# Performance work log

Measured on AMD Instinct MI355X. Metric: run time of the kernel, lower is better.

The kernel has to match this reference:

```python
import jax, jax.numpy as jnp
import numpy as np


def _dequantize_int4(qweight, scales, qzeros, blocksize):
    """Unpack int4 weights (two nibbles per byte along N) and dequantize.

    qweight: [K, N/2] int (byte values 0..255); low nibble = even col, high nibble = odd col
    scales:  [groups, N] float32, groups = K // blocksize
    qzeros:  [groups, N/2] int (packed like qweight)
    returns: [K, N] float32 dequantized weight, w = (q - z) * s per group along K
    """
    K, Nh = qweight.shape
    N = Nh * 2
    groups = scales.shape[0]
    low = (qweight & 0xF).astype(jnp.float32)
    high = ((qweight >> 4) & 0xF).astype(jnp.float32)
    wq = jnp.stack([low, high], axis=-1).reshape(K, N)  # [K, N]
    zl = (qzeros & 0xF).astype(jnp.float32)
    zh = ((qzeros >> 4) & 0xF).astype(jnp.float32)
    zq = jnp.stack([zl, zh], axis=-1).reshape(groups, N)  # [groups, N]
    # group-wise dequant along K without materializing repeated scale/zero tables
    w = (wq.reshape(groups, blocksize, N) - zq[:, None, :]) * scales[:, None, :]
    return w.reshape(K, N)


def setup_inputs() -> dict:
    key = jax.random.key(0)
    k1, k2, k3, k4, k5 = jax.random.split(key, 5)
    B, S, K = 32, 64, 4096
    N_PAD = 32064
    BLOCKSIZE = 128
    GROUPS = K // BLOCKSIZE
    x = jax.random.normal(k1, (B, S, K), dtype=jnp.float32)
    qweight = jax.random.randint(k2, (K, N_PAD // 2), 0, 256, dtype=jnp.int32)
    scales = jax.random.uniform(k3, (GROUPS, N_PAD), dtype=jnp.float32) * 0.02 + 1e-3
    qzeros = jax.random.randint(k4, (GROUPS, N_PAD // 2), 0, 256, dtype=jnp.int32)
    bias = jax.random.normal(k5, (N_PAD,), dtype=jnp.float32) * 0.01
    return {"x": x, "qweight": qweight, "scales": scales, "qzeros": qzeros,
            "bias": bias, "blocksize": BLOCKSIZE, "n_dim": 32000}


def reference(x, qweight, scales, qzeros, bias, blocksize, n_dim):
    # mimic module.forward with acc_test=False: keep only the last token
    if x.ndim > 3:
        x = x.reshape(-1, x.shape[-2], x.shape[-1])
    x_last = x[:, -1:, :]  # [B, 1, K]
    w = _dequantize_int4(qweight, scales, qzeros, blocksize)  # [K, N_pad]
    out = jnp.einsum('bsk,kn->bsn', x_last, w) + bias  # mm_bias_int4
    return out[:, :, :n_dim]  # strip vocab padding
```

## Files before the change

kernel.cpp:

```cpp
#include <hip/hip_runtime.h>
#include <hip/hip_bf16.h>


typedef _Float16 f16x8 __attribute__((ext_vector_type(8)));
typedef _Float16 f16x2 __attribute__((ext_vector_type(2)));
typedef float f32x4 __attribute__((ext_vector_type(4)));

#define K_DIM 4096
#define NP 16032
#define NSC 32064
#define NOUT 32000
#define S_LEN 64
#define QROWB ((size_t)NP * 4)
#define QSTEP (32u * (uint32_t)NP * 4u)

__global__ void prep_a_kernel(const float* __restrict__ x,
                              _Float16* __restrict__ aws) {
    int tid = blockIdx.x * 256 + threadIdx.x;
    int l = tid & 63;
    int mblk = (tid >> 6) & 1;
    int ks = tid >> 7;
    int m = mblk * 16 + (l & 15);
    int kbase = ks * 32 + 8 * (l >> 4);
    const float* xp = x + (size_t)m * S_LEN * K_DIM + (size_t)(S_LEN - 1) * K_DIM + kbase;
    _Float16* op = aws + (size_t)tid * 8;
#pragma unroll
    for (int j = 0; j < 8; ++j) op[j] = (_Float16)xp[j];
}

__device__ __forceinline__ int f16pk(int w0, int w1, int sh2) {
    int e0 = (w0 >> sh2) & 15;
    int e1 = (w1 >> sh2) & 15;
    return e0 | (e1 << 16) | 0x64006400;
}

__global__ __launch_bounds__(512, 4)
void q4gemm_kernel(const int* __restrict__ qw,
                   const float* __restrict__ scales,
                   const int* __restrict__ qzeros,
                   const float* __restrict__ bias,
                   const _Float16* __restrict__ aws,
                   float* __restrict__ out) {
    __shared__ float red[8 * 2048];

    const int tid = threadIdx.x;
    const int w = tid >> 6;
    const int l = tid & 63;
    const int h = l >> 4;
    const int c = l & 15;
    const int n0 = blockIdx.x * 64;
    const int np0 = n0 >> 1;

    const char* qwb = (const char*)qw;
    uint32_t qoff = (uint32_t)((w * 512 + 8 * h) * (size_t)NP + np0 + 2 * c) * 4u;

    f32x4 acc0[4] = {};
    f32x4 acc1[4] = {};
    f16x2 vz[4], vs[4];

    int2 qa[8], qb[8];

#define QLD(buf)                                                              \
    do {                                                                      \
        _Pragma("unroll") for (int j = 0; j < 8; ++j)                         \
            buf[j] = *(const int2*)(qwb + qoff + (size_t)j * QROWB);          \
        qoff += QSTEP;                                                        \
    } while (0)

#define GRPUPD(g)                                                             \
    do {                                                                      \
        f32x4 sc4 = *(const f32x4*)(scales + (size_t)(g) * NSC + n0 + 4 * c); \
        int2 zw = *(const int2*)(qzeros + (size_t)(g) * NP + np0 + 2 * c);    \
        _Pragma("unroll") for (int s = 0; s < 4; ++s) {                       \
            int zword = (s < 2) ? zw.x : zw.y;                                \
            int z = (zword >> ((s & 1) * 4)) & 15;                            \
            int zp = z | (z << 16) | 0x64006400;                              \
            vz[s] = __builtin_bit_cast(f16x2, zp);                            \
            _Float16 sh_ = (_Float16)sc4[s];                                  \
            f16x2 sp = {sh_, sh_};                                            \
            vs[s] = sp;                                                       \
        }                                                                     \
    } while (0)

#define COMPUTE(buf, ksg)                                                     \
    do {                                                                      \
        f16x8 a0 = *(const f16x8*)(aws + ((size_t)((ksg) * 2 + 0) * 64 + l) * 8); \
        f16x8 a1 = *(const f16x8*)(aws + ((size_t)((ksg) * 2 + 1) * 64 + l) * 8); \
        _Pragma("unroll") for (int s = 0; s < 4; ++s) {                       \
            const int sh2 = (s & 1) * 4;                                      \
            int4 bi;                                                          \
            _Pragma("unroll") for (int p = 0; p < 4; ++p) {                   \
                int w0 = (s < 2) ? buf[2 * p].x : buf[2 * p].y;               \
                int w1 = (s < 2) ? buf[2 * p + 1].x : buf[2 * p + 1].y;       \
                f16x2 vq = __builtin_bit_cast(f16x2, f16pk(w0, w1, sh2));     \
                f16x2 r = (vq - vz[s]) * vs[s];                               \
                bi[p] = __builtin_bit_cast(int, r);                           \
            }                                                                 \
            f16x8 b = __builtin_bit_cast(f16x8, bi);                          \
            acc0[s] = __builtin_amdgcn_mfma_f32_16x16x32_f16(a0, b, acc0[s], 0, 0, 0); \
            acc1[s] = __builtin_amdgcn_mfma_f32_16x16x32_f16(a1, b, acc1[s], 0, 0, 0); \
        }                                                                     \
    } while (0)

    QLD(qa);
#pragma unroll
    for (int tt = 0; tt < 8; ++tt) {
        const int t0 = 2 * tt;
        QLD(qb);
        if ((tt & 1) == 0) GRPUPD(w * 4 + tt / 2);
        COMPUTE(qa, w * 16 + t0);
        if (tt < 7) QLD(qa);
        COMPUTE(qb, w * 16 + t0 + 1);
    }

#pragma unroll
    for (int s = 0; s < 4; ++s)
#pragma unroll
        for (int r = 0; r < 4; ++r) {
            red[w * 2048 + (h * 4 + r) * 64 + 4 * c + s] = acc0[s][r];
            red[w * 2048 + (16 + h * 4 + r) * 64 + 4 * c + s] = acc1[s][r];
        }

    __syncthreads();

#pragma unroll
    for (int i = 0; i < 4; ++i) {
        int e = i * 512 + tid;
        float sum = 0.f;
#pragma unroll
        for (int ww = 0; ww < 8; ++ww) sum += red[ww * 2048 + e];
        int m = e >> 6;
        int n = n0 + (e & 63);
        out[(size_t)m * NOUT + n] = sum + bias[n];
    }
}

extern "C" void kernel_launch(void* const* d_in, const int* in_sizes, int n_in,
                              void* d_out, int out_size, void* d_ws, size_t ws_size,
                              hipStream_t stream) {
    const float* x       = (const float*)d_in[0];
    const int*   qweight = (const int*)d_in[1];
    const float* scales  = (const float*)d_in[2];
    const int*   qzeros  = (const int*)d_in[3];
    const float* bias    = (const float*)d_in[4];

    _Float16* aws = (_Float16*)d_ws;
    float* out = (float*)d_out;

    prep_a_kernel<<<64, 256, 0, stream>>>(x, aws);
    q4gemm_kernel<<<500, 512, 0, stream>>>(qweight, scales, qzeros, bias, aws, out);
}
```

Before: 50.16 us.

## Fuse activation fp16 conversion into GEMM kernel and use nontemporal weight loads

Drops the separate prep kernel that converted the last-token activations to fp16 in a workspace. Each GEMM wave now loads the fp32 activations directly and converts them in registers, saving one kernel launch and a workspace round trip. Weight, scale and zero loads are switched to nontemporal loads so the streamed weights do not pollute the cache. The cost is that all 500 blocks re-read and re-convert the fp32 activations, which doubles activation bytes per load and adds conversion instructions.

```diff
diff --git a/kernel.cpp b/kernel.cpp
--- a/kernel.cpp
+++ b/kernel.cpp
@@ -5,6 +5,7 @@
 typedef _Float16 f16x8 __attribute__((ext_vector_type(8)));
 typedef _Float16 f16x2 __attribute__((ext_vector_type(2)));
 typedef float f32x4 __attribute__((ext_vector_type(4)));
+typedef int i32x2 __attribute__((ext_vector_type(2)));
 
 #define K_DIM 4096
 #define NP 16032
@@ -14,32 +15,12 @@
 #define QROWB ((size_t)NP * 4)
 #define QSTEP (32u * (uint32_t)NP * 4u)
 
-__global__ void prep_a_kernel(const float* __restrict__ x,
-                              _Float16* __restrict__ aws) {
-    int tid = blockIdx.x * 256 + threadIdx.x;
-    int l = tid & 63;
-    int mblk = (tid >> 6) & 1;
-    int ks = tid >> 7;
-    int m = mblk * 16 + (l & 15);
-    int kbase = ks * 32 + 8 * (l >> 4);
-    const float* xp = x + (size_t)m * S_LEN * K_DIM + (size_t)(S_LEN - 1) * K_DIM + kbase;
-    _Float16* op = aws + (size_t)tid * 8;
-#pragma unroll
-    for (int j = 0; j < 8; ++j) op[j] = (_Float16)xp[j];
-}
-
-__device__ __forceinline__ int f16pk(int w0, int w1, int sh2) {
-    int e0 = (w0 >> sh2) & 15;
-    int e1 = (w1 >> sh2) & 15;
-    return e0 | (e1 << 16) | 0x64006400;
-}
-
 __global__ __launch_bounds__(512, 4)
-void q4gemm_kernel(const int* __restrict__ qw,
+void q4gemm_kernel(const float* __restrict__ x,
+                   const int* __restrict__ qw,
                    const float* __restrict__ scales,
                    const int* __restrict__ qzeros,
                    const float* __restrict__ bias,
-                   const _Float16* __restrict__ aws,
                    float* __restrict__ out) {
     __shared__ float red[8 * 2048];
 
@@ -54,25 +35,31 @@
     const char* qwb = (const char*)qw;
     uint32_t qoff = (uint32_t)((w * 512 + 8 * h) * (size_t)NP + np0 + 2 * c) * 4u;
 
+    const float* xr0 = x + ((size_t)c * S_LEN + (S_LEN - 1)) * K_DIM;
+    const float* xr1 = x + ((size_t)(16 + c) * S_LEN + (S_LEN - 1)) * K_DIM;
+
     f32x4 acc0[4] = {};
     f32x4 acc1[4] = {};
     f16x2 vz[4], vs[4];
 
-    int2 qa[8], qb[8];
+    i32x2 qa[8], qb[8];
 
 #define QLD(buf)                                                              \
     do {                                                                      \
         _Pragma("unroll") for (int j = 0; j < 8; ++j)                         \
-            buf[j] = *(const int2*)(qwb + qoff + (size_t)j * QROWB);          \
+            buf[j] = __builtin_nontemporal_load(                              \
+                (const i32x2*)(qwb + qoff + (size_t)j * QROWB));              \
         qoff += QSTEP;                                                        \
     } while (0)
 
 #define GRPUPD(g)                                                             \
     do {                                                                      \
-        f32x4 sc4 = *(const f32x4*)(scales + (size_t)(g) * NSC + n0 + 4 * c); \
-        int2 zw = *(const int2*)(qzeros + (size_t)(g) * NP + np0 + 2 * c);    \
+        f32x4 sc4 = __builtin_nontemporal_load(                               \
+            (const f32x4*)(scales + (size_t)(g) * NSC + n0 + 4 * c));         \
+        i32x2 zw = __builtin_nontemporal_load(                                \
+            (const i32x2*)(qzeros + (size_t)(g) * NP + np0 + 2 * c));         \
         _Pragma("unroll") for (int s = 0; s < 4; ++s) {                       \
-            int zword = (s < 2) ? zw.x : zw.y;                                \
+            int zword = (s < 2) ? zw[0] : zw[1];                              \
             int z = (zword >> ((s & 1) * 4)) & 15;                            \
             int zp = z | (z << 16) | 0x64006400;                              \
             vz[s] = __builtin_bit_cast(f16x2, zp);                            \
@@ -82,17 +69,32 @@
         }                                                                     \
     } while (0)
 
+#define AFRAG(dst, xr, koff)                                                  \
+    do {                                                                      \
+        f32x4 u0 = *(const f32x4*)((xr) + (koff));                            \
+        f32x4 u1 = *(const f32x4*)((xr) + (koff) + 4);                        \
+        _Pragma("unroll") for (int j = 0; j < 4; ++j) {                       \
+            dst[j] = (_Float16)u0[j];                                         \
+            dst[4 + j] = (_Float16)u1[j];                                     \
+        }                                                                     \
+    } while (0)
+
 #define COMPUTE(buf, ksg)                                                     \
     do {                                                                      \
-        f16x8 a0 = *(const f16x8*)(aws + ((size_t)((ksg) * 2 + 0) * 64 + l) * 8); \
-        f16x8 a1 = *(const f16x8*)(aws + ((size_t)((ksg) * 2 + 1) * 64 + l) * 8); \
+        const int koff = (ksg) * 32 + 8 * h;                                  \
+        f16x8 a0, a1;                                                         \
+        AFRAG(a0, xr0, koff);                                                 \
+        AFRAG(a1, xr1, koff);                                                 \
         _Pragma("unroll") for (int s = 0; s < 4; ++s) {                       \
             const int sh2 = (s & 1) * 4;                                      \
             int4 bi;                                                          \
             _Pragma("unroll") for (int p = 0; p < 4; ++p) {                   \
-                int w0 = (s < 2) ? buf[2 * p].x : buf[2 * p].y;               \
-                int w1 = (s < 2) ? buf[2 * p + 1].x : buf[2 * p + 1].y;       \
-                f16x2 vq = __builtin_bit_cast(f16x2, f16pk(w0, w1, sh2));     \
+                int w0 = (s < 2) ? buf[2 * p][0] : buf[2 * p][1];             \
+                int w1 = (s < 2) ? buf[2 * p + 1][0] : buf[2 * p + 1][1];     \
+                int e0 = (w0 >> sh2) & 15;                                    \
+                int e1 = (w1 >> sh2) & 15;                                    \
+                int pk = e0 | (e1 << 16) | 0x64006400;                        \
+                f16x2 vq = __builtin_bit_cast(f16x2, pk);                     \
                 f16x2 r = (vq - vz[s]) * vs[s];                               \
                 bi[p] = __builtin_bit_cast(int, r);                           \
             }                                                                 \
@@ -143,10 +145,7 @@
     const float* scales  = (const float*)d_in[2];
     const int*   qzeros  = (const int*)d_in[3];
     const float* bias    = (const float*)d_in[4];
-
-    _Float16* aws = (_Float16*)d_ws;
     float* out = (float*)d_out;
 
-    prep_a_kernel<<<64, 256, 0, stream>>>(x, aws);
-    q4gemm_kernel<<<500, 512, 0, stream>>>(qweight, scales, qzeros, bias, aws, out);
+    q4gemm_kernel<<<500, 512, 0, stream>>>(x, qweight, scales, qzeros, bias, out);
 }
```

Measured after the change: 64.31 us. 28.2% more time.
